# Performance work log

Hardware: AMD Instinct MI355X
Metric: run time of the kernel (lower is better)

## Reference

```python
import jax, jax.numpy as jnp
import numpy as np

N = 2048          # num instances
L = 16            # num labels
SIGMA = 1.0       # learn2rank_sigma
EPS = 1e-10


def setup_inputs() -> dict:
    key = jax.random.key(0)
    k1, k2, k3 = jax.random.split(key, 3)
    inp = jax.random.normal(k1, (N, L), dtype=jnp.float32)
    target = jax.random.randint(k2, (N, L), 0, 2).astype(jnp.float32)  # binary labels
    label_weights = jax.random.uniform(k3, (L,), dtype=jnp.float32)
    return {"input": inp, "target": target, "label_weights": label_weights}


def reference(input, target, label_weights):
    n, num_labels = input.shape
    # all i<j pairs, vectorized (replaces the O(N^2) python loop of torch.stack calls)
    ii, jj = jnp.triu_indices(n, k=1)          # [P], P = n*(n-1)/2
    o_ij = jnp.clip(input[ii] - input[jj], -50.0, 50.0)                 # [P, L]
    p_tgt = jnp.clip(0.5 * (1.0 + target[ii] - target[jj]), EPS, 1.0 - EPS)  # [P, L]
    mask = p_tgt != 0.5                          # pairs with differing labels
    o_s = o_ij * SIGMA
    # RankNet loss: -p*o + log(1 + exp(o)), weighted per label
    per_pair = (-p_tgt * o_s + jnp.log1p(jnp.exp(o_s))) * label_weights  # [P, L]
    loss = jnp.sum(jnp.where(mask, per_pair, 0.0))
    return loss / num_labels
```

## Files before the change

kernel.cpp:

```cpp
#include <hip/hip_runtime.h>
#include <math.h>

#define NN 2048
#define LL 16
#define EPSF 1e-10f

static constexpr int TNT  = 6;
static constexpr int TPC  = 10;
static constexpr int SLOT = TNT * TPC;
static constexpr int GRP  = 4;
static constexpr int BPL  = SLOT / GRP;
static constexpr int NBLK = LL * BPL;
static constexpr float LOG2E = 1.44269504088896340736f;


__global__ __launch_bounds__(1024) void fused_kernel(
    const float* __restrict__ inp, const float* __restrict__ tgt,
    double* __restrict__ partial, double* __restrict__ corr)
{
    const int gid = blockIdx.x;
    const int L   = gid / BPL;
    const int rem = gid % BPL;
    const int tid = threadIdx.x;
    const int lane = tid & 63, wid = tid >> 6;

    __shared__ float posL[NN];
    __shared__ float negL[NN];
    __shared__ unsigned wco[16];
    __shared__ double red[16];

    const int r0 = tid * 2;
    const float s0 = inp[(size_t)r0 * LL + L];
    const float s1 = inp[(size_t)(r0 + 1) * LL + L];
    const int tg0 = (tgt[(size_t)r0 * LL + L] != 0.0f) ? 1 : 0;
    const int tg1 = (tgt[(size_t)(r0 + 1) * LL + L] != 0.0f) ? 1 : 0;

    const int lpos = tg0 + tg1, lneg = 2 - lpos;
    const unsigned pk = (unsigned)lpos | ((unsigned)lneg << 16);
    unsigned ipk = pk;
#pragma unroll
    for (int off = 1; off < 64; off <<= 1) {
        const unsigned tu = __shfl_up(ipk, off, 64);
        if (lane >= off) ipk += tu;
    }
    if (lane == 63) wco[wid] = ipk;
    __syncthreads();

    unsigned basec = 0;
    for (int w = 0; w < wid; ++w) basec += wco[w];
    unsigned totc = 0;
#pragma unroll
    for (int w = 0; w < 16; ++w) totc += wco[w];
    const int npos = (int)(totc & 0xffffu);
    const int nneg = (int)(totc >> 16);
    const int nchunkP = (npos + 127) >> 7;
    const int ntileN  = (nneg + 255) >> 8;

    const int grp  = tid >> 8;
    const int slot = rem * GRP + grp;
    const int nt = slot / TPC, pc = slot % TPC;
    const bool myvalid = (nt < ntileN) && (pc < nchunkP);
    {
        const int s0v = rem * GRP;
        bool anyv = false;
#pragma unroll
        for (int g = 0; g < GRP; ++g) {
            const int sl = s0v + g;
            anyv = anyv || ((sl / TPC) < ntileN && (sl % TPC) < nchunkP);
        }
        if (!anyv && rem != 0) {
            if (tid == 0) partial[gid] = 0.0;
            return;
        }
    }

    const unsigned exc = basec + ipk - pk;
    int rp = (int)(exc & 0xffffu);
    int rn = (int)(exc >> 16);

    const bool docorr = (rem == 0);
    double cl = 0.0;
    if (tg0) { posL[rp] = s0 * LOG2E; if (docorr) cl += (double)rn * (double)s0; ++rp; }
    else     { negL[rn] = s0 * LOG2E; if (docorr) cl -= (double)(npos - rp) * (double)s0; ++rn; }
    if (tg1) { posL[rp] = s1 * LOG2E; if (docorr) cl += (double)rn * (double)s1; ++rp; }
    else     { negL[rn] = s1 * LOG2E; if (docorr) cl -= (double)(npos - rp) * (double)s1; ++rn; }

    if (docorr) {
#pragma unroll
        for (int off = 32; off > 0; off >>= 1)
            cl += __shfl_down(cl, off, 64);
        if (lane == 0) red[wid] = cl;
    }

    const int posP = (npos + 127) & ~127;
    const int negP = (nneg + 255) & ~255;
    for (int idx = npos + tid; idx < posP; idx += 1024) posL[idx] =  1e30f;
    for (int idx = nneg + tid; idx < negP; idx += 1024) negL[idx] = -1e30f;
    __syncthreads();

    if (docorr && tid == 0) {
        double c = 0.0;
#pragma unroll
        for (int w = 0; w < 16; ++w) c += red[w];
        corr[L] = c;
    }
    if (docorr) __syncthreads();

    const int t256 = tid & 255;
    double acc = 0.0;
    if (myvalid) {
        const float nv = negL[nt * 256 + t256];
        const float4* p4 = (const float4*)(posL + pc * 128);
#pragma unroll
        for (int r = 0; r < 32; ++r) {
            const float4 pv = p4[r];
            const float e0 = __builtin_amdgcn_exp2f(nv - pv.x);
            const float e1 = __builtin_amdgcn_exp2f(nv - pv.y);
            const float e2 = __builtin_amdgcn_exp2f(nv - pv.z);
            const float e3 = __builtin_amdgcn_exp2f(nv - pv.w);
            const float P = ((1.0f + e0) * (1.0f + e1)) * ((1.0f + e2) * (1.0f + e3));
            acc += (double)__log2f(P);
        }
    }

#pragma unroll
    for (int off = 32; off > 0; off >>= 1)
        acc += __shfl_down(acc, off, 64);
    if (lane == 0) red[wid] = acc;
    __syncthreads();
    if (tid == 0) {
        double a = 0.0;
#pragma unroll
        for (int w = 0; w < 16; ++w) a += red[w];
        partial[gid] = a;
    }
}

__global__ __launch_bounds__(256) void final_kernel(
    const double* __restrict__ partial, const double* __restrict__ corr,
    const float* __restrict__ lw, float* __restrict__ out)
{
    const int tid = threadIdx.x;
    const double LN2 = 0.69314718055994530942;

    double acc = 0.0;
    if (tid < NBLK)
        acc = (double)lw[tid / BPL] * (LN2 * partial[tid]);
    if (tid < LL)
        acc += (double)lw[tid] * ((double)EPSF * corr[tid]);

    const int lane = tid & 63, wid = tid >> 6;
#pragma unroll
    for (int off = 32; off > 0; off >>= 1)
        acc += __shfl_down(acc, off, 64);
    __shared__ double smem[4];
    if (lane == 0) smem[wid] = acc;
    __syncthreads();
    if (tid == 0)
        out[0] = (float)((smem[0] + smem[1] + smem[2] + smem[3]) / (double)LL);
}

extern "C" void kernel_launch(void* const* d_in, const int* in_sizes, int n_in,
                              void* d_out, int out_size, void* d_ws, size_t ws_size,
                              hipStream_t stream) {
    const float* inp = (const float*)d_in[0];
    const float* tgt = (const float*)d_in[1];
    const float* lw  = (const float*)d_in[2];
    float* out = (float*)d_out;

    char* ws = (char*)d_ws;
    double* partial = (double*)(ws);
    double* corr    = (double*)(ws + 1920);

    fused_kernel<<<NBLK, 1024, 0, stream>>>(inp, tgt, partial, corr);
    final_kernel<<<1, 256, 0, stream>>>(partial, corr, lw, out);
}
```

Baseline: 16.74 us.

## Fuse final reduction into main kernel via completion flags

Drops the separate final_kernel launch. Each block publishes a magic completion flag and then checks whether all 240 block flags are set; a block that sees every flag performs the weighted final reduction and writes the output, then clears the flags. The aim is to remove the second kernel launch and its dependency gap. In exchange, blocks with no work no longer exit early, several blocks may redundantly finalize, and correctness depends on the flag workspace not already holding the magic value.

```diff
diff --git a/kernel.cpp b/kernel.cpp
--- a/kernel.cpp
+++ b/kernel.cpp
@@ -12,11 +12,14 @@
 static constexpr int BPL  = SLOT / GRP;
 static constexpr int NBLK = LL * BPL;
 static constexpr float LOG2E = 1.44269504088896340736f;
+static constexpr unsigned MAGIC = 0x5EED5EEDu;
 
 
 __global__ __launch_bounds__(1024) void fused_kernel(
     const float* __restrict__ inp, const float* __restrict__ tgt,
-    double* __restrict__ partial, double* __restrict__ corr)
+    const float* __restrict__ lw,
+    double* __restrict__ partial, double* __restrict__ corr,
+    unsigned* __restrict__ flags, float* __restrict__ out)
 {
     const int gid = blockIdx.x;
     const int L   = gid / BPL;
@@ -28,6 +31,7 @@
     __shared__ float negL[NN];
     __shared__ unsigned wco[16];
     __shared__ double red[16];
+    __shared__ int okgate;
 
     const int r0 = tid * 2;
     const float s0 = inp[(size_t)r0 * LL + L];
@@ -60,66 +64,65 @@
     const int slot = rem * GRP + grp;
     const int nt = slot / TPC, pc = slot % TPC;
     const bool myvalid = (nt < ntileN) && (pc < nchunkP);
+    bool anyv = false;
     {
         const int s0v = rem * GRP;
-        bool anyv = false;
 #pragma unroll
         for (int g = 0; g < GRP; ++g) {
             const int sl = s0v + g;
             anyv = anyv || ((sl / TPC) < ntileN && (sl % TPC) < nchunkP);
         }
-        if (!anyv && rem != 0) {
-            if (tid == 0) partial[gid] = 0.0;
-            return;
-        }
-    }
-
-    const unsigned exc = basec + ipk - pk;
-    int rp = (int)(exc & 0xffffu);
-    int rn = (int)(exc >> 16);
-
-    const bool docorr = (rem == 0);
-    double cl = 0.0;
-    if (tg0) { posL[rp] = s0 * LOG2E; if (docorr) cl += (double)rn * (double)s0; ++rp; }
-    else     { negL[rn] = s0 * LOG2E; if (docorr) cl -= (double)(npos - rp) * (double)s0; ++rn; }
-    if (tg1) { posL[rp] = s1 * LOG2E; if (docorr) cl += (double)rn * (double)s1; ++rp; }
-    else     { negL[rn] = s1 * LOG2E; if (docorr) cl -= (double)(npos - rp) * (double)s1; ++rn; }
-
-    if (docorr) {
-#pragma unroll
-        for (int off = 32; off > 0; off >>= 1)
-            cl += __shfl_down(cl, off, 64);
-        if (lane == 0) red[wid] = cl;
-    }
-
-    const int posP = (npos + 127) & ~127;
-    const int negP = (nneg + 255) & ~255;
-    for (int idx = npos + tid; idx < posP; idx += 1024) posL[idx] =  1e30f;
-    for (int idx = nneg + tid; idx < negP; idx += 1024) negL[idx] = -1e30f;
-    __syncthreads();
-
-    if (docorr && tid == 0) {
-        double c = 0.0;
-#pragma unroll
-        for (int w = 0; w < 16; ++w) c += red[w];
-        corr[L] = c;
-    }
-    if (docorr) __syncthreads();
-
-    const int t256 = tid & 255;
+    }
+    const bool skipwork = (!anyv && rem != 0);
+
     double acc = 0.0;
-    if (myvalid) {
-        const float nv = negL[nt * 256 + t256];
-        const float4* p4 = (const float4*)(posL + pc * 128);
-#pragma unroll
-        for (int r = 0; r < 32; ++r) {
-            const float4 pv = p4[r];
-            const float e0 = __builtin_amdgcn_exp2f(nv - pv.x);
-            const float e1 = __builtin_amdgcn_exp2f(nv - pv.y);
-            const float e2 = __builtin_amdgcn_exp2f(nv - pv.z);
-            const float e3 = __builtin_amdgcn_exp2f(nv - pv.w);
-            const float P = ((1.0f + e0) * (1.0f + e1)) * ((1.0f + e2) * (1.0f + e3));
-            acc += (double)__log2f(P);
+    if (!skipwork) {
+        const unsigned exc = basec + ipk - pk;
+        int rp = (int)(exc & 0xffffu);
+        int rn = (int)(exc >> 16);
+
+        const bool docorr = (rem == 0);
+        double cl = 0.0;
+        if (tg0) { posL[rp] = s0 * LOG2E; if (docorr) cl += (double)rn * (double)s0; ++rp; }
+        else     { negL[rn] = s0 * LOG2E; if (docorr) cl -= (double)(npos - rp) * (double)s0; ++rn; }
+        if (tg1) { posL[rp] = s1 * LOG2E; if (docorr) cl += (double)rn * (double)s1; ++rp; }
+        else     { negL[rn] = s1 * LOG2E; if (docorr) cl -= (double)(npos - rp) * (double)s1; ++rn; }
+
+        if (docorr) {
+#pragma unroll
+            for (int off = 32; off > 0; off >>= 1)
+                cl += __shfl_down(cl, off, 64);
+            if (lane == 0) red[wid] = cl;
+        }
+
+        const int posP = (npos + 127) & ~127;
+        const int negP = (nneg + 255) & ~255;
+        for (int idx = npos + tid; idx < posP; idx += 1024) posL[idx] =  1e30f;
+        for (int idx = nneg + tid; idx < negP; idx += 1024) negL[idx] = -1e30f;
+        __syncthreads();
+
+        if (docorr && tid == 0) {
+            double c = 0.0;
+#pragma unroll
+            for (int w = 0; w < 16; ++w) c += red[w];
+            corr[L] = c;
+        }
+        if (docorr) __syncthreads();
+
+        const int t256 = tid & 255;
+        if (myvalid) {
+            const float nv = negL[nt * 256 + t256];
+            const float4* p4 = (const float4*)(posL + pc * 128);
+#pragma unroll
+            for (int r = 0; r < 32; ++r) {
+                const float4 pv = p4[r];
+                const float e0 = __builtin_amdgcn_exp2f(nv - pv.x);
+                const float e1 = __builtin_amdgcn_exp2f(nv - pv.y);
+                const float e2 = __builtin_amdgcn_exp2f(nv - pv.z);
+                const float e3 = __builtin_amdgcn_exp2f(nv - pv.w);
+                const float P = ((1.0f + e0) * (1.0f + e1)) * ((1.0f + e2) * (1.0f + e3));
+                acc += (double)__log2f(P);
+            }
         }
     }
 
@@ -134,30 +137,51 @@
         for (int w = 0; w < 16; ++w) a += red[w];
         partial[gid] = a;
     }
-}
-
-__global__ __launch_bounds__(256) void final_kernel(
-    const double* __restrict__ partial, const double* __restrict__ corr,
-    const float* __restrict__ lw, float* __restrict__ out)
-{
-    const int tid = threadIdx.x;
+
+    if (tid == 0) {
+        __hip_atomic_store(&flags[(size_t)gid * 16], MAGIC,
+                           __ATOMIC_RELEASE, __HIP_MEMORY_SCOPE_AGENT);
+        __threadfence();
+    }
+    __syncthreads();
+
+    int ok = 1;
+    if (tid < NBLK)
+        ok = (__hip_atomic_load(&flags[(size_t)tid * 16],
+                                __ATOMIC_RELAXED, __HIP_MEMORY_SCOPE_AGENT) == MAGIC);
+    ok = __all(ok) ? 1 : 0;
+    if (lane == 0) wco[wid] = (unsigned)ok;
+    __syncthreads();
+    if (tid == 0) {
+        unsigned A = 1;
+#pragma unroll
+        for (int w = 0; w < 16; ++w) A &= wco[w];
+        okgate = (int)A;
+    }
+    __syncthreads();
+    if (!okgate) return;
+
+    __threadfence();
+    if (tid >= 256) return;
+
     const double LN2 = 0.69314718055994530942;
-
-    double acc = 0.0;
+    double f = 0.0;
     if (tid < NBLK)
-        acc = (double)lw[tid / BPL] * (LN2 * partial[tid]);
+        f = (double)lw[tid / BPL] * (LN2 * partial[tid]);
     if (tid < LL)
-        acc += (double)lw[tid] * ((double)EPSF * corr[tid]);
-
-    const int lane = tid & 63, wid = tid >> 6;
+        f += (double)lw[tid] * ((double)EPSF * corr[tid]);
+
 #pragma unroll
     for (int off = 32; off > 0; off >>= 1)
-        acc += __shfl_down(acc, off, 64);
-    __shared__ double smem[4];
-    if (lane == 0) smem[wid] = acc;
+        f += __shfl_down(f, off, 64);
+    if (lane == 0) red[wid] = f;
     __syncthreads();
     if (tid == 0)
-        out[0] = (float)((smem[0] + smem[1] + smem[2] + smem[3]) / (double)LL);
+        out[0] = (float)(((((red[0] + red[1]) + red[2]) + red[3])) / (double)LL);
+
+    if (tid < NBLK)
+        __hip_atomic_store(&flags[(size_t)tid * 16], 0u,
+                           __ATOMIC_RELAXED, __HIP_MEMORY_SCOPE_AGENT);
 }
 
 extern "C" void kernel_launch(void* const* d_in, const int* in_sizes, int n_in,
@@ -169,9 +193,9 @@
     float* out = (float*)d_out;
 
     char* ws = (char*)d_ws;
-    double* partial = (double*)(ws);
-    double* corr    = (double*)(ws + 1920);
-
-    fused_kernel<<<NBLK, 1024, 0, stream>>>(inp, tgt, partial, corr);
-    final_kernel<<<1, 256, 0, stream>>>(partial, corr, lw, out);
+    double*   partial = (double*)(ws);
+    double*   corr    = (double*)(ws + 1920);
+    unsigned* flags   = (unsigned*)(ws + 2048);
+
+    fused_kernel<<<NBLK, 1024, 0, stream>>>(inp, tgt, lw, partial, corr, flags, out);
 }
```

Result: slower. 43.50 us (+159.9%).
